# Kernel tuning notes

Hardware: AMD Instinct MI355X
Metric: run time of the kernel (lower is better)

Reference implementation:

```python
import jax, jax.numpy as jnp
import numpy as np

B, N, E, H = 8, 512, 256, 8
HD = E // H
FF = 4 * E
TOPK = max(1, int(N * 0.2))
FW_MAX_DIST = 10      # default of get_shortest_path_matrix
EMB_MAX_IDX = 6       # spd encoder: max_dist(5) + 1
LN_EPS = 1e-5


def _layernorm(x, g, b):
    m = jnp.mean(x, axis=-1, keepdims=True)
    v = jnp.var(x, axis=-1, keepdims=True)
    return (x - m) / jnp.sqrt(v + LN_EPS) * g + b


def setup_inputs() -> dict:
    key = jax.random.key(0)
    ks = jax.random.split(key, 12)
    s = 0.02
    return {
        "x": jax.random.normal(ks[0], (B, N, E), jnp.float32),
        "adj": jax.random.uniform(ks[1], (B, N, N), jnp.float32),
        "emb_spd": (jax.random.normal(ks[2], (EMB_MAX_IDX + 1, H), jnp.float32) * s),
        "w_qkv": jax.random.normal(ks[3], (3 * E, E), jnp.float32) * s,
        "b_qkv": jnp.zeros((3 * E,), jnp.float32),
        "w_out": jax.random.normal(ks[4], (E, E), jnp.float32) * s,
        "b_out": jnp.zeros((E,), jnp.float32),
        "w_ff1": jax.random.normal(ks[5], (FF, E), jnp.float32) * s,
        "b_ff1": jnp.zeros((FF,), jnp.float32),
        "w_ff2": jax.random.normal(ks[6], (E, FF), jnp.float32) * s,
        "b_ff2": jnp.zeros((E,), jnp.float32),
        "g1": jnp.ones((E,), jnp.float32),
        "beta1": jnp.zeros((E,), jnp.float32),
        "g2": jnp.ones((E,), jnp.float32),
        "beta2": jnp.zeros((E,), jnp.float32),
        "w_pool": jax.random.normal(ks[7], (1, E), jnp.float32) * s,
        "b_pool": jnp.zeros((1,), jnp.float32),
    }


def _combined_mask(adj, emb_spd):
    # top-k per row -> binary adjacency via scatter
    _, idx = jax.lax.top_k(adj, TOPK)                       # [B,N,k]
    bi = jnp.arange(B)[:, None, None]
    ri = jnp.arange(N)[None, :, None]
    binary = jnp.zeros_like(adj).at[bi, ri, idx].set(1.0)   # [B,N,N]

    # Floyd-Warshall shortest paths
    dist = jnp.where(binary == 1.0, 1.0, jnp.inf)
    ids = jnp.arange(N)
    dist = dist.at[:, ids, ids].set(0.0)

    def body(k, d):
        return jnp.minimum(d, d[:, :, k][:, :, None] + d[:, k, :][:, None, :])

    dist = jax.lax.fori_loop(0, N, body, dist)
    dist_i = jnp.where(dist > FW_MAX_DIST, -1.0, dist).astype(jnp.int32)

    # spatial bias embedding: indices = clamp(dist+1, 0, max_dist+1)
    sp_idx = jnp.clip(dist_i + 1, 0, EMB_MAX_IDX)           # [B,N,N]
    bias = jnp.transpose(emb_spd[sp_idx], (0, 3, 1, 2))     # [B,H,N,N]

    base = jnp.where(binary == 0.0, -jnp.inf, 0.0)[:, None] # [B,1,N,N]
    return base + bias                                      # [B,H,N,N]


def reference(x, adj, emb_spd, w_qkv, b_qkv, w_out, b_out,
              w_ff1, b_ff1, w_ff2, b_ff2, g1, beta1, g2, beta2,
              w_pool, b_pool):
    mask = _combined_mask(adj, emb_spd)                     # [B,H,N,N]

    # multi-head self-attention (PyTorch MHA, post-norm encoder layer, eval)
    qkv = x @ w_qkv.T + b_qkv                               # [B,N,3E]
    q, k, v = jnp.split(qkv, 3, axis=-1)
    q = q.reshape(B, N, H, HD).transpose(0, 2, 1, 3)
    k = k.reshape(B, N, H, HD).transpose(0, 2, 1, 3)
    v = v.reshape(B, N, H, HD).transpose(0, 2, 1, 3)
    scores = jnp.einsum("bhqd,bhkd->bhqk", q, k) / np.sqrt(HD) + mask
    attn = jax.nn.softmax(scores, axis=-1)
    ctx = jnp.einsum("bhqk,bhkd->bhqd", attn, v)
    ctx = ctx.transpose(0, 2, 1, 3).reshape(B, N, E)
    attn_out = ctx @ w_out.T + b_out

    x1 = _layernorm(x + attn_out, g1, beta1)
    ff = jax.nn.relu(x1 @ w_ff1.T + b_ff1) @ w_ff2.T + b_ff2
    x2 = _layernorm(x1 + ff, g2, beta2)

    # attention pooling over nodes
    w = jax.nn.softmax(jnp.tanh(x2 @ w_pool.T + b_pool), axis=1)  # [B,N,1]
    return jnp.sum(x2 * w, axis=1)                          # [B,E]
```

## Files before the change

kernel.cpp:

```cpp
#include <hip/hip_runtime.h>
#include <math.h>


#define B_ 8
#define N_ 512
#define E_ 256
#define H_ 8
#define HD_ 32
#define TOPK_ 102

typedef __attribute__((ext_vector_type(8))) short bf16x8;
typedef __attribute__((ext_vector_type(4))) float f32x4;

__device__ __forceinline__ unsigned short f2b(float f) {
  unsigned u = __builtin_bit_cast(unsigned, f);
  return (unsigned short)((u + 0x7FFFu + ((u >> 16) & 1u)) >> 16);
}

__global__ __launch_bounds__(256) void cvt_all(
    const float* __restrict__ x, const float* __restrict__ wqkv,
    const float* __restrict__ wout, const float* __restrict__ wff1,
    const float* __restrict__ wff2, unsigned short* __restrict__ xb,
    unsigned short* __restrict__ wqkvb, unsigned short* __restrict__ woutb,
    unsigned short* __restrict__ wff1b, unsigned short* __restrict__ wff2b) {
  int i = (blockIdx.x * 256 + threadIdx.x) * 4;
  const float* src;
  unsigned short* dst;
  int off;
  if (i < 1048576)      { src = x;    dst = xb;    off = i; }
  else if (i < 1245184) { src = wqkv; dst = wqkvb; off = i - 1048576; }
  else if (i < 1310720) { src = wout; dst = woutb; off = i - 1245184; }
  else if (i < 1572864) { src = wff1; dst = wff1b; off = i - 1310720; }
  else                  { src = wff2; dst = wff2b; off = i - 1572864; }
  float4 v = *(const float4*)(src + off);
  ushort4 o;
  o.x = f2b(v.x); o.y = f2b(v.y); o.z = f2b(v.z); o.w = f2b(v.w);
  *(ushort4*)(dst + off) = o;
}

__global__ __launch_bounds__(256) void topk_kernel(const float* __restrict__ adj,
                                                   unsigned int* __restrict__ bits) {
  const int row = blockIdx.x;
  const float* a = adj + (size_t)row * N_;
  __shared__ unsigned int hist[1024];
  __shared__ float cval[N_];
  __shared__ int cidx[N_];
  __shared__ int s_cnt;
  __shared__ int s_bb;
  __shared__ int s_need;
  __shared__ unsigned int rowbits[16];
  __shared__ int wsum[4];
  const int t = threadIdx.x;
  const int lane = t & 63;
  const int wave = t >> 6;

  hist[t] = 0u; hist[t + 256] = 0u; hist[t + 512] = 0u; hist[t + 768] = 0u;
  if (t == 0) s_cnt = 0;
  float v0 = a[t];
  float v1 = a[t + 256];
  __syncthreads();
  const int b0 = min(1023, max(0, (int)(v0 * 1024.0f)));
  const int b1 = min(1023, max(0, (int)(v1 * 1024.0f)));
  atomicAdd(&hist[b0], 1u);
  atomicAdd(&hist[b1], 1u);
  __syncthreads();
  const int base = 1020 - 4 * t;
  const int h0 = (int)hist[base], h1 = (int)hist[base + 1];
  const int h2 = (int)hist[base + 2], h3 = (int)hist[base + 3];
  const int g = h0 + h1 + h2 + h3;
  int sc = g;
  #pragma unroll
  for (int off = 1; off < 64; off <<= 1) {
    int y = __shfl_up(sc, off);
    sc += (lane >= off) ? y : 0;
  }
  if (lane == 63) wsum[wave] = sc;
  __syncthreads();
  int wo = 0;
  for (int w = 0; w < wave; w++) wo += wsum[w];
  const int incl = sc + wo;
  const int excl = incl - g;
  if (excl < TOPK_ && incl >= TOPK_) {
    int cum = excl;
    int bb = base;
    const int hh[4] = {h3, h2, h1, h0};
    const int bs[4] = {base + 3, base + 2, base + 1, base};
    #pragma unroll
    for (int u = 0; u < 4; u++) {
      if (cum + hh[u] >= TOPK_) { bb = bs[u]; break; }
      cum += hh[u];
    }
    s_bb = bb;
    s_need = TOPK_ - cum;
  }
  __syncthreads();
  const int bb = s_bb;
  const int need = s_need;
  const bool sel0 = (b0 > bb);
  const bool sel1 = (b1 > bb);
  if (b0 == bb) { int p = atomicAdd(&s_cnt, 1); cval[p] = v0; cidx[p] = t; }
  if (b1 == bb) { int p = atomicAdd(&s_cnt, 1); cval[p] = v1; cidx[p] = t + 256; }
  unsigned long long m0 = __ballot(sel0);
  unsigned long long m1 = __ballot(sel1);
  if (lane == 0) {
    rowbits[2 * wave + 0] = (unsigned int)m0;
    rowbits[2 * wave + 1] = (unsigned int)(m0 >> 32);
    rowbits[8 + 2 * wave + 0] = (unsigned int)m1;
    rowbits[8 + 2 * wave + 1] = (unsigned int)(m1 >> 32);
  }
  __syncthreads();
  const int cnt = s_cnt;
  for (int c = t; c < cnt; c += 256) {
    const float v = cval[c];
    const int idx = cidx[c];
    int r = 0;
    for (int j = 0; j < cnt; j++) {
      const float vj = cval[j];
      const int ij = cidx[j];
      if (vj > v || (vj == v && ij < idx)) r++;
    }
    if (r < need) atomicOr(&rowbits[idx >> 5], 1u << (idx & 31));
  }
  __syncthreads();
  if (t < 16) bits[(size_t)row * 16 + t] = rowbits[t];
}

__global__ __launch_bounds__(256) void gemm_mfma(
    const unsigned short* __restrict__ A, const unsigned short* __restrict__ W,
    const float* __restrict__ bias, const float* __restrict__ res,
    void* __restrict__ Cout, int M, int N, int K, int flags) {
  __shared__ __align__(16) unsigned short Af[8 * 64 * 8];
  __shared__ __align__(16) unsigned short Wf[8 * 64 * 8];
  const int tid = threadIdx.x;
  const int m0 = blockIdx.y * 64, n0 = blockIdx.x * 64;
  const int wave = tid >> 6, lane = tid & 63;
  const int wm = wave & 1, wn = wave >> 1;
  const int q = lane >> 4, l15 = lane & 15;
  const int r = tid >> 2, c0 = tid & 3;

  f32x4 acc[2][2];
  #pragma unroll
  for (int i = 0; i < 2; i++)
    #pragma unroll
    for (int j = 0; j < 2; j++) acc[i][j] = (f32x4){0.f, 0.f, 0.f, 0.f};

  const size_t arow = (size_t)(m0 + r) * K;
  const size_t wrow = (size_t)(n0 + r) * K;
  for (int k0 = 0; k0 < K; k0 += 64) {
    uint4 a0 = *(const uint4*)(A + arow + k0 + c0 * 8);
    uint4 a1 = *(const uint4*)(A + arow + k0 + (c0 + 4) * 8);
    uint4 w0 = *(const uint4*)(W + wrow + k0 + c0 * 8);
    uint4 w1 = *(const uint4*)(W + wrow + k0 + (c0 + 4) * 8);
    __syncthreads();
    {
      int kc = c0 >> 2, qq = c0 & 3;
      int s0 = ((r >> 4) * 2 + kc) * 64 + (r & 15) + qq * 16;
      int kc1 = (c0 + 4) >> 2, qq1 = (c0 + 4) & 3;
      int s1 = ((r >> 4) * 2 + kc1) * 64 + (r & 15) + qq1 * 16;
      *(uint4*)(Af + s0 * 8) = a0;
      *(uint4*)(Af + s1 * 8) = a1;
      *(uint4*)(Wf + s0 * 8) = w0;
      *(uint4*)(Wf + s1 * 8) = w1;
    }
    __syncthreads();
    #pragma unroll
    for (int kc = 0; kc < 2; kc++) {
      bf16x8 af[2], wf[2];
      #pragma unroll
      for (int mt = 0; mt < 2; mt++)
        af[mt] = *(const bf16x8*)(Af + (((wm * 2 + mt) * 2 + kc) * 64 + lane) * 8);
      #pragma unroll
      for (int nt = 0; nt < 2; nt++)
        wf[nt] = *(const bf16x8*)(Wf + (((wn * 2 + nt) * 2 + kc) * 64 + lane) * 8);
      #pragma unroll
      for (int mt = 0; mt < 2; mt++)
        #pragma unroll
        for (int nt = 0; nt < 2; nt++)
          acc[mt][nt] = __builtin_amdgcn_mfma_f32_16x16x32_bf16(af[mt], wf[nt], acc[mt][nt], 0, 0, 0);
    }
  }
  #pragma unroll
  for (int nt = 0; nt < 2; nt++) {
    const int col = n0 + (wn * 2 + nt) * 16 + l15;
    const float bv = bias[col];
    #pragma unroll
    for (int mt = 0; mt < 2; mt++) {
      const int rowb = m0 + (wm * 2 + mt) * 16 + q * 4;
      #pragma unroll
      for (int reg = 0; reg < 4; reg++) {
        const int row = rowb + reg;
        float o = acc[mt][nt][reg] + bv;
        if (res) o += res[(size_t)row * N + col];
        if (flags & 1) o = fmaxf(o, 0.f);
        if (flags & 2) ((unsigned short*)Cout)[(size_t)row * N + col] = f2b(o);
        else           ((float*)Cout)[(size_t)row * N + col] = o;
      }
    }
  }
}

__global__ __launch_bounds__(256) void attn_mfma(
    const unsigned short* __restrict__ qkv, const unsigned int* __restrict__ bits,
    const float* __restrict__ emb, unsigned short* __restrict__ ctxo) {
  const int bx = blockIdx.x;
  const int ib = bx & 7;
  const int h = (bx >> 3) & 7;
  const int b = bx >> 6;
  const int tid = threadIdx.x;
  const int lane = tid & 63;
  const int wave = tid >> 6;
  const int q = lane >> 4, l15 = lane & 15;

  __shared__ __align__(16) unsigned short kF[4 * 64 * 8];
  __shared__ __align__(16) unsigned short vF[4 * 64 * 8];
  __shared__ __align__(16) unsigned int mrow[64 * 16];
  __shared__ __align__(16) unsigned short pF[4][2 * 64 * 8];

  {
    int rr = tid >> 2, wq = tid & 3;
    uint4 mw = *(const uint4*)(bits + ((size_t)(b * N_ + ib * 64 + rr)) * 16 + wq * 4);
    *(uint4*)(mrow + rr * 16 + wq * 4) = mw;
  }
  const int i0w = ib * 64 + wave * 16;
  const bf16x8 qf = *(const bf16x8*)(qkv + ((size_t)(b * N_ + i0w + l15)) * 768 + h * HD_ + q * 8);
  const float delta = emb[1 * H_ + h] - emb[2 * H_ + h];
  const float scale = 0.17677669529663687f;

  float m_run[4], l_run[4];
  #pragma unroll
  for (int e = 0; e < 4; e++) { m_run[e] = -1e30f; l_run[e] = 0.f; }
  f32x4 cacc[2];
  cacc[0] = (f32x4){0.f, 0.f, 0.f, 0.f};
  cacc[1] = (f32x4){0.f, 0.f, 0.f, 0.f};

  unsigned short* pbase = &pF[wave][0];
  const int sj = tid >> 2, scb = tid & 3;

  #pragma unroll 1
  for (int jt = 0; jt < 8; jt++) {
    __syncthreads();
    {
      const unsigned short* kvrow = qkv + ((size_t)(b * N_ + jt * 64 + sj)) * 768 + h * HD_;
      uint4 kv4 = *(const uint4*)(kvrow + E_ + scb * 8);
      *(uint4*)(kF + (((sj >> 4) * 64) + (sj & 15) + scb * 16) * 8) = kv4;
      uint4 vv4 = *(const uint4*)(kvrow + 2 * E_ + scb * 8);
      const unsigned short* vp = (const unsigned short*)&vv4;
      #pragma unroll
      for (int e2 = 0; e2 < 8; e2++) {
        int d = scb * 8 + e2;
        int slot = ((d >> 4) * 2 + (sj >> 5)) * 64 + (d & 15) + ((sj >> 3) & 3) * 16;
        vF[slot * 8 + (sj & 7)] = vp[e2];
      }
    }
    __syncthreads();
    f32x4 s4[4];
    #pragma unroll
    for (int jtile = 0; jtile < 4; jtile++) {
      bf16x8 kf = *(const bf16x8*)(kF + (jtile * 64 + lane) * 8);
      s4[jtile] = __builtin_amdgcn_mfma_f32_16x16x32_bf16(qf, kf, (f32x4){0.f, 0.f, 0.f, 0.f}, 0, 0, 0);
    }
    unsigned long long mw64[4];
    #pragma unroll
    for (int reg = 0; reg < 4; reg++)
      mw64[reg] = *(const unsigned long long*)(mrow + (wave * 16 + q * 4 + reg) * 16 + jt * 2);
    float smat[4][4];
    #pragma unroll
    for (int jtile = 0; jtile < 4; jtile++) {
      #pragma unroll
      for (int reg = 0; reg < 4; reg++) {
        unsigned int w = (jtile & 2) ? (unsigned int)(mw64[reg] >> 32) : (unsigned int)mw64[reg];
        bool allowed = ((w >> ((jtile & 1) * 16 + l15)) & 1u) != 0u;
        int ig = ib * 64 + wave * 16 + q * 4 + reg;
        int jg = jt * 64 + jtile * 16 + l15;
        float s = s4[jtile][reg] * scale + ((jg == ig) ? delta : 0.f);
        smat[jtile][reg] = allowed ? s : -INFINITY;
      }
    }
    float alpha[4], pmat[4][4];
    #pragma unroll
    for (int reg = 0; reg < 4; reg++) {
      float mloc = fmaxf(fmaxf(smat[0][reg], smat[1][reg]), fmaxf(smat[2][reg], smat[3][reg]));
      #pragma unroll
      for (int off = 1; off < 16; off <<= 1) mloc = fmaxf(mloc, __shfl_xor(mloc, off));
      float mnew = fmaxf(m_run[reg], mloc);
      alpha[reg] = __expf(m_run[reg] - mnew);
      m_run[reg] = mnew;
      float ps = 0.f;
      #pragma unroll
      for (int jtile = 0; jtile < 4; jtile++) {
        float p = __expf(smat[jtile][reg] - mnew);
        pmat[jtile][reg] = p;
        ps += p;
      }
      #pragma unroll
      for (int off = 1; off < 16; off <<= 1) ps += __shfl_xor(ps, off);
      l_run[reg] = l_run[reg] * alpha[reg] + ps;
      cacc[0][reg] *= alpha[reg];
      cacc[1][reg] *= alpha[reg];
    }
    #pragma unroll
    for (int jtile = 0; jtile < 4; jtile++) {
      int j_l = jtile * 16 + l15;
      int sl = ((j_l >> 5) * 64 + ((j_l >> 3) & 3) * 16) * 8 + (j_l & 7);
      #pragma unroll
      for (int reg = 0; reg < 4; reg++)
        pbase[sl + (q * 4 + reg) * 8] = f2b(pmat[jtile][reg]);
    }
    #pragma unroll
    for (int kc = 0; kc < 2; kc++) {
      bf16x8 pf = *(const bf16x8*)(pbase + (kc * 64 + lane) * 8);
      #pragma unroll
      for (int dt = 0; dt < 2; dt++) {
        bf16x8 vf = *(const bf16x8*)(vF + ((dt * 2 + kc) * 64 + lane) * 8);
        cacc[dt] = __builtin_amdgcn_mfma_f32_16x16x32_bf16(pf, vf, cacc[dt], 0, 0, 0);
      }
    }
  }
  #pragma unroll
  for (int reg = 0; reg < 4; reg++) {
    const float linv = 1.f / l_run[reg];
    const size_t row = (size_t)(b * N_ + i0w + q * 4 + reg);
    #pragma unroll
    for (int dt = 0; dt < 2; dt++)
      ctxo[row * E_ + h * HD_ + dt * 16 + l15] = f2b(cacc[dt][reg] * linv);
  }
}

__global__ __launch_bounds__(256) void layernorm_kernel(
    const float* __restrict__ t, const float* __restrict__ g,
    const float* __restrict__ be, float* __restrict__ out,
    unsigned short* __restrict__ outb, const float* __restrict__ wp,
    const float* __restrict__ bp, float* __restrict__ ew) {
  const int row = blockIdx.x;
  const int tid = threadIdx.x;
  float v = t[(size_t)row * E_ + tid];
  float s = v, s2 = v * v;
  #pragma unroll
  for (int off = 32; off > 0; off >>= 1) {
    s += __shfl_xor(s, off);
    s2 += __shfl_xor(s2, off);
  }
  __shared__ float sh[8];
  const int wave = tid >> 6, lane = tid & 63;
  if (lane == 0) { sh[wave] = s; sh[4 + wave] = s2; }
  __syncthreads();
  s = sh[0] + sh[1] + sh[2] + sh[3];
  s2 = sh[4] + sh[5] + sh[6] + sh[7];
  float mean = s * (1.f / 256.f);
  float var = s2 * (1.f / 256.f) - mean * mean;
  float inv = rsqrtf(var + 1e-5f);
  float o = (v - mean) * inv * g[tid] + be[tid];
  out[(size_t)row * E_ + tid] = o;
  if (outb) outb[(size_t)row * E_ + tid] = f2b(o);
  if (ew) {
    float d = o * wp[tid];
    #pragma unroll
    for (int off = 32; off > 0; off >>= 1) d += __shfl_xor(d, off);
    __syncthreads();
    if (lane == 0) sh[wave] = d;
    __syncthreads();
    if (tid == 0) {
      float dot = sh[0] + sh[1] + sh[2] + sh[3] + bp[0];
      ew[row] = __expf(tanhf(dot));
    }
  }
}

__global__ __launch_bounds__(256) void pool_partial(
    const float* __restrict__ x2, const float* __restrict__ ew,
    float* __restrict__ partial, float* __restrict__ pwsum) {
  const int c = blockIdx.x;
  const int b = blockIdx.y;
  const int tid = threadIdx.x;
  const int r0 = b * N_ + c * 16;
  float acc = 0.f;
  #pragma unroll
  for (int n = 0; n < 16; n++)
    acc += ew[r0 + n] * x2[(size_t)(r0 + n) * E_ + tid];
  partial[(size_t)(b * 32 + c) * E_ + tid] = acc;
  if (tid < 16) {
    float w = ew[r0 + tid];
    #pragma unroll
    for (int off = 1; off < 16; off <<= 1) w += __shfl_xor(w, off);
    if (tid == 0) pwsum[b * 32 + c] = w;
  }
}

__global__ __launch_bounds__(256) void pool_final(
    const float* __restrict__ partial, const float* __restrict__ pwsum,
    float* __restrict__ out) {
  const int b = blockIdx.x;
  const int tid = threadIdx.x;
  float acc = 0.f, ws = 0.f;
  #pragma unroll
  for (int c = 0; c < 32; c++) acc += partial[(size_t)(b * 32 + c) * E_ + tid];
  #pragma unroll
  for (int c = 0; c < 32; c++) ws += pwsum[b * 32 + c];
  out[b * E_ + tid] = acc / ws;
}

extern "C" void kernel_launch(void* const* d_in, const int* in_sizes, int n_in,
                              void* d_out, int out_size, void* d_ws, size_t ws_size,
                              hipStream_t stream) {
  (void)in_sizes; (void)n_in; (void)out_size; (void)ws_size;
  const float* x      = (const float*)d_in[0];
  const float* adj    = (const float*)d_in[1];
  const float* emb    = (const float*)d_in[2];
  const float* w_qkv  = (const float*)d_in[3];
  const float* b_qkv  = (const float*)d_in[4];
  const float* w_out  = (const float*)d_in[5];
  const float* b_out  = (const float*)d_in[6];
  const float* w_ff1  = (const float*)d_in[7];
  const float* b_ff1  = (const float*)d_in[8];
  const float* w_ff2  = (const float*)d_in[9];
  const float* b_ff2  = (const float*)d_in[10];
  const float* g1     = (const float*)d_in[11];
  const float* be1    = (const float*)d_in[12];
  const float* g2     = (const float*)d_in[13];
  const float* be2    = (const float*)d_in[14];
  const float* w_pool = (const float*)d_in[15];
  const float* b_pool = (const float*)d_in[16];

  char* ws = (char*)d_ws;
  unsigned int*   bits  = (unsigned int*)ws;
  unsigned short* xb    = (unsigned short*)(ws + 262144);
  unsigned short* qkvb  = (unsigned short*)(ws + 2359296);
  unsigned short* hffb  = xb;
  unsigned short* ctxb  = (unsigned short*)(ws + 8650752);
  unsigned short* x1b   = (unsigned short*)(ws + 10747904);
  unsigned short* wqkvb = (unsigned short*)(ws + 12845056);
  unsigned short* woutb = (unsigned short*)(ws + 13238272);
  unsigned short* wff1b = (unsigned short*)(ws + 13369344);
  unsigned short* wff2b = (unsigned short*)(ws + 13893632);
  float*          tbuf  = (float*)(ws + 14417920);
  float*          x1    = (float*)(ws + 18612224);
  float*          x2    = (float*)(ws + 22806528);
  float*          ew      = (float*)(ws + 8650752);
  float*          partial = (float*)(ws + 8650752 + 16384);
  float*          pwsum   = (float*)(ws + 8650752 + 16384 + 262144);
  float*          outp  = (float*)d_out;

  const int M = B_ * N_;

  cvt_all<<<1835008 / 1024, 256, 0, stream>>>(x, w_qkv, w_out, w_ff1, w_ff2,
                                              xb, wqkvb, woutb, wff1b, wff2b);
  topk_kernel<<<B_ * N_, 256, 0, stream>>>(adj, bits);
  gemm_mfma<<<dim3(768 / 64, M / 64), 256, 0, stream>>>(
      xb, wqkvb, b_qkv, nullptr, qkvb, M, 768, E_, 2);
  attn_mfma<<<B_ * H_ * (N_ / 64), 256, 0, stream>>>(qkvb, bits, emb, ctxb);
  gemm_mfma<<<dim3(E_ / 64, M / 64), 256, 0, stream>>>(
      ctxb, woutb, b_out, x, tbuf, M, E_, E_, 0);
  layernorm_kernel<<<M, 256, 0, stream>>>(tbuf, g1, be1, x1, x1b,
                                          nullptr, nullptr, nullptr);
  gemm_mfma<<<dim3(1024 / 64, M / 64), 256, 0, stream>>>(
      x1b, wff1b, b_ff1, nullptr, hffb, M, 1024, E_, 1 | 2);
  gemm_mfma<<<dim3(E_ / 64, M / 64), 256, 0, stream>>>(
      hffb, wff2b, b_ff2, x1, tbuf, M, E_, 1024, 0);
  layernorm_kernel<<<M, 256, 0, stream>>>(tbuf, g2, be2, x2, nullptr,
                                          w_pool, b_pool, ew);
  pool_partial<<<dim3(32, 8), 256, 0, stream>>>(x2, ew, partial, pwsum);
  pool_final<<<B_, 256, 0, stream>>>(partial, pwsum, outp);
}
```

Measured before the change: 179.8 us.

## Fuse out-proj and FF2 GEMMs with layernorm; write transposed V from QKV GEMM

Replaces the out-projection and FF2 GEMMs and their separate layernorm kernels with a fused gemm_ln kernel. Each block computes 16 full rows of 256 columns with MFMA, reading operands straight from global memory, then does the row layernorm and pooling-weight dot in registers and shared memory. This removes the fp32 tbuf round trip and two kernel launches. The QKV GEMM now also writes V in a transposed per-head layout, so attention reads K and V fragments directly from global memory and drops its shared-memory staging and per-tile barriers. The trade-off is no LDS reuse in gemm_ln, only 256 small blocks, and more global-load traffic in attention.

```diff
diff --git a/kernel.cpp b/kernel.cpp
--- a/kernel.cpp
+++ b/kernel.cpp
@@ -128,7 +128,8 @@
 __global__ __launch_bounds__(256) void gemm_mfma(
     const unsigned short* __restrict__ A, const unsigned short* __restrict__ W,
     const float* __restrict__ bias, const float* __restrict__ res,
-    void* __restrict__ Cout, int M, int N, int K, int flags) {
+    void* __restrict__ Cout, unsigned short* __restrict__ vT,
+    int M, int N, int K, int flags) {
   __shared__ __align__(16) unsigned short Af[8 * 64 * 8];
   __shared__ __align__(16) unsigned short Wf[8 * 64 * 8];
   const int tid = threadIdx.x;
@@ -186,22 +187,35 @@
     #pragma unroll
     for (int mt = 0; mt < 2; mt++) {
       const int rowb = m0 + (wm * 2 + mt) * 16 + q * 4;
+      float ov[4];
       #pragma unroll
       for (int reg = 0; reg < 4; reg++) {
-        const int row = rowb + reg;
         float o = acc[mt][nt][reg] + bv;
-        if (res) o += res[(size_t)row * N + col];
+        if (res) o += res[(size_t)(rowb + reg) * N + col];
         if (flags & 1) o = fmaxf(o, 0.f);
-        if (flags & 2) ((unsigned short*)Cout)[(size_t)row * N + col] = f2b(o);
-        else           ((float*)Cout)[(size_t)row * N + col] = o;
+        ov[reg] = o;
       }
+      if (vT && col >= 512) {
+        const int d = (col - 512) & 31, hh2 = (col - 512) >> 5;
+        const int bidx = rowb >> 9, j0 = rowb & 511;
+        ushort4 st;
+        st.x = f2b(ov[0]); st.y = f2b(ov[1]); st.z = f2b(ov[2]); st.w = f2b(ov[3]);
+        *(ushort4*)(vT + ((size_t)((bidx * 8 + hh2) * 32 + d)) * 512 + j0) = st;
+      } else {
+        #pragma unroll
+        for (int reg = 0; reg < 4; reg++) {
+          if (flags & 2) ((unsigned short*)Cout)[(size_t)(rowb + reg) * N + col] = f2b(ov[reg]);
+          else           ((float*)Cout)[(size_t)(rowb + reg) * N + col] = ov[reg];
+        }
+      }
     }
   }
 }
 
 __global__ __launch_bounds__(256) void attn_mfma(
-    const unsigned short* __restrict__ qkv, const unsigned int* __restrict__ bits,
-    const float* __restrict__ emb, unsigned short* __restrict__ ctxo) {
+    const unsigned short* __restrict__ qkv, const unsigned short* __restrict__ vT,
+    const unsigned int* __restrict__ bits, const float* __restrict__ emb,
+    unsigned short* __restrict__ ctxo) {
   const int bx = blockIdx.x;
   const int ib = bx & 7;
   const int h = (bx >> 3) & 7;
@@ -211,8 +225,6 @@
   const int wave = tid >> 6;
   const int q = lane >> 4, l15 = lane & 15;
 
-  __shared__ __align__(16) unsigned short kF[4 * 64 * 8];
-  __shared__ __align__(16) unsigned short vF[4 * 64 * 8];
   __shared__ __align__(16) unsigned int mrow[64 * 16];
   __shared__ __align__(16) unsigned short pF[4][2 * 64 * 8];
 
@@ -221,6 +233,8 @@
     uint4 mw = *(const uint4*)(bits + ((size_t)(b * N_ + ib * 64 + rr)) * 16 + wq * 4);
     *(uint4*)(mrow + rr * 16 + wq * 4) = mw;
   }
+  __syncthreads();
+
   const int i0w = ib * 64 + wave * 16;
   const bf16x8 qf = *(const bf16x8*)(qkv + ((size_t)(b * N_ + i0w + l15)) * 768 + h * HD_ + q * 8);
   const float delta = emb[1 * H_ + h] - emb[2 * H_ + h];
@@ -234,29 +248,15 @@
   cacc[1] = (f32x4){0.f, 0.f, 0.f, 0.f};
 
   unsigned short* pbase = &pF[wave][0];
-  const int sj = tid >> 2, scb = tid & 3;
+  const unsigned short* kbase = qkv + (size_t)b * N_ * 768 + E_ + h * HD_ + q * 8;
+  const unsigned short* vbase = vT + ((size_t)((b * 8 + h) * 32 + l15)) * 512 + q * 8;
 
   #pragma unroll 1
   for (int jt = 0; jt < 8; jt++) {
-    __syncthreads();
-    {
-      const unsigned short* kvrow = qkv + ((size_t)(b * N_ + jt * 64 + sj)) * 768 + h * HD_;
-      uint4 kv4 = *(const uint4*)(kvrow + E_ + scb * 8);
-      *(uint4*)(kF + (((sj >> 4) * 64) + (sj & 15) + scb * 16) * 8) = kv4;
-      uint4 vv4 = *(const uint4*)(kvrow + 2 * E_ + scb * 8);
-      const unsigned short* vp = (const unsigned short*)&vv4;
-      #pragma unroll
-      for (int e2 = 0; e2 < 8; e2++) {
-        int d = scb * 8 + e2;
-        int slot = ((d >> 4) * 2 + (sj >> 5)) * 64 + (d & 15) + ((sj >> 3) & 3) * 16;
-        vF[slot * 8 + (sj & 7)] = vp[e2];
-      }
-    }
-    __syncthreads();
     f32x4 s4[4];
     #pragma unroll
     for (int jtile = 0; jtile < 4; jtile++) {
-      bf16x8 kf = *(const bf16x8*)(kF + (jtile * 64 + lane) * 8);
+      bf16x8 kf = *(const bf16x8*)(kbase + (size_t)(jt * 64 + jtile * 16 + l15) * 768);
       s4[jtile] = __builtin_amdgcn_mfma_f32_16x16x32_bf16(qf, kf, (f32x4){0.f, 0.f, 0.f, 0.f}, 0, 0, 0);
     }
     unsigned long long mw64[4];
@@ -311,7 +311,7 @@
       bf16x8 pf = *(const bf16x8*)(pbase + (kc * 64 + lane) * 8);
       #pragma unroll
       for (int dt = 0; dt < 2; dt++) {
-        bf16x8 vf = *(const bf16x8*)(vF + ((dt * 2 + kc) * 64 + lane) * 8);
+        bf16x8 vf = *(const bf16x8*)(vbase + (size_t)dt * 16 * 512 + jt * 64 + kc * 32);
         cacc[dt] = __builtin_amdgcn_mfma_f32_16x16x32_bf16(pf, vf, cacc[dt], 0, 0, 0);
       }
     }
@@ -326,42 +326,91 @@
   }
 }
 
-__global__ __launch_bounds__(256) void layernorm_kernel(
-    const float* __restrict__ t, const float* __restrict__ g,
-    const float* __restrict__ be, float* __restrict__ out,
-    unsigned short* __restrict__ outb, const float* __restrict__ wp,
-    const float* __restrict__ bp, float* __restrict__ ew) {
-  const int row = blockIdx.x;
+__global__ __launch_bounds__(256) void gemm_ln(
+    const unsigned short* __restrict__ A, const unsigned short* __restrict__ W,
+    const float* __restrict__ bias, const float* __restrict__ res,
+    const float* __restrict__ g, const float* __restrict__ be,
+    float* __restrict__ xout, unsigned short* __restrict__ xbout,
+    const float* __restrict__ wp, const float* __restrict__ bp,
+    float* __restrict__ ew, int K) {
   const int tid = threadIdx.x;
-  float v = t[(size_t)row * E_ + tid];
-  float s = v, s2 = v * v;
-  #pragma unroll
-  for (int off = 32; off > 0; off >>= 1) {
-    s += __shfl_xor(s, off);
-    s2 += __shfl_xor(s2, off);
-  }
-  __shared__ float sh[8];
-  const int wave = tid >> 6, lane = tid & 63;
-  if (lane == 0) { sh[wave] = s; sh[4 + wave] = s2; }
-  __syncthreads();
-  s = sh[0] + sh[1] + sh[2] + sh[3];
-  s2 = sh[4] + sh[5] + sh[6] + sh[7];
-  float mean = s * (1.f / 256.f);
-  float var = s2 * (1.f / 256.f) - mean * mean;
-  float inv = rsqrtf(var + 1e-5f);
-  float o = (v - mean) * inv * g[tid] + be[tid];
-  out[(size_t)row * E_ + tid] = o;
-  if (outb) outb[(size_t)row * E_ + tid] = f2b(o);
+  const int wv = tid >> 6, lane = tid & 63;
+  const int q = lane >> 4, l15 = lane & 15;
+  const int m0 = blockIdx.x * 16;
+  f32x4 acc[4];
+  #pragma unroll
+  for (int nt = 0; nt < 4; nt++) acc[nt] = (f32x4){0.f, 0.f, 0.f, 0.f};
+
+  const unsigned short* ap = A + (size_t)(m0 + l15) * K + q * 8;
+  const unsigned short* wr = W + (size_t)(wv * 64 + l15) * K + q * 8;
+  const int K32 = K >> 5;
+  for (int kc = 0; kc < K32; kc++) {
+    bf16x8 af = *(const bf16x8*)(ap + kc * 32);
+    #pragma unroll
+    for (int nt = 0; nt < 4; nt++) {
+      bf16x8 wf = *(const bf16x8*)(wr + (size_t)nt * 16 * K + kc * 32);
+      acc[nt] = __builtin_amdgcn_mfma_f32_16x16x32_bf16(af, wf, acc[nt], 0, 0, 0);
+    }
+  }
+  __shared__ float rs[16][4], rs2[16][4];
+  float o[4][4];
+  int cols[4];
+  #pragma unroll
+  for (int nt = 0; nt < 4; nt++) cols[nt] = wv * 64 + nt * 16 + l15;
+  #pragma unroll
+  for (int reg = 0; reg < 4; reg++) {
+    const int row = m0 + q * 4 + reg;
+    float p = 0.f, p2 = 0.f;
+    #pragma unroll
+    for (int nt = 0; nt < 4; nt++) {
+      float v = acc[nt][reg] + bias[cols[nt]];
+      if (res) v += res[(size_t)row * 256 + cols[nt]];
+      o[nt][reg] = v;
+      p += v; p2 += v * v;
+    }
+    #pragma unroll
+    for (int off = 1; off < 16; off <<= 1) {
+      p += __shfl_xor(p, off);
+      p2 += __shfl_xor(p2, off);
+    }
+    if (l15 == 0) { rs[q * 4 + reg][wv] = p; rs2[q * 4 + reg][wv] = p2; }
+  }
+  __syncthreads();
+  #pragma unroll
+  for (int reg = 0; reg < 4; reg++) {
+    const int r = q * 4 + reg;
+    float s = rs[r][0] + rs[r][1] + rs[r][2] + rs[r][3];
+    float s2 = rs2[r][0] + rs2[r][1] + rs2[r][2] + rs2[r][3];
+    float mean = s * (1.f / 256.f);
+    float var = s2 * (1.f / 256.f) - mean * mean;
+    float inv = rsqrtf(var + 1e-5f);
+    #pragma unroll
+    for (int nt = 0; nt < 4; nt++) {
+      float on = (o[nt][reg] - mean) * inv * g[cols[nt]] + be[cols[nt]];
+      o[nt][reg] = on;
+      xout[(size_t)(m0 + r) * 256 + cols[nt]] = on;
+      if (xbout) xbout[(size_t)(m0 + r) * 256 + cols[nt]] = f2b(on);
+    }
+  }
   if (ew) {
-    float d = o * wp[tid];
-    #pragma unroll
-    for (int off = 32; off > 0; off >>= 1) d += __shfl_xor(d, off);
     __syncthreads();
-    if (lane == 0) sh[wave] = d;
+    #pragma unroll
+    for (int reg = 0; reg < 4; reg++) {
+      float d = 0.f;
+      #pragma unroll
+      for (int nt = 0; nt < 4; nt++) d += o[nt][reg] * wp[cols[nt]];
+      #pragma unroll
+      for (int off = 1; off < 16; off <<= 1) d += __shfl_xor(d, off);
+      if (l15 == 0) rs[q * 4 + reg][wv] = d;
+    }
     __syncthreads();
-    if (tid == 0) {
-      float dot = sh[0] + sh[1] + sh[2] + sh[3] + bp[0];
-      ew[row] = __expf(tanhf(dot));
+    if (wv == 0 && l15 == 0) {
+      #pragma unroll
+      for (int reg = 0; reg < 4; reg++) {
+        const int r = q * 4 + reg;
+        float dot = rs[r][0] + rs[r][1] + rs[r][2] + rs[r][3] + bp[0];
+        ew[m0 + r] = __expf(tanhf(dot));
+      }
     }
   }
 }
@@ -432,7 +481,7 @@
   unsigned short* woutb = (unsigned short*)(ws + 13238272);
   unsigned short* wff1b = (unsigned short*)(ws + 13369344);
   unsigned short* wff2b = (unsigned short*)(ws + 13893632);
-  float*          tbuf  = (float*)(ws + 14417920);
+  unsigned short* vTb   = (unsigned short*)(ws + 14417920);
   float*          x1    = (float*)(ws + 18612224);
   float*          x2    = (float*)(ws + 22806528);
   float*          ew      = (float*)(ws + 8650752);
@@ -446,18 +495,14 @@
                                               xb, wqkvb, woutb, wff1b, wff2b);
   topk_kernel<<<B_ * N_, 256, 0, stream>>>(adj, bits);
   gemm_mfma<<<dim3(768 / 64, M / 64), 256, 0, stream>>>(
-      xb, wqkvb, b_qkv, nullptr, qkvb, M, 768, E_, 2);
-  attn_mfma<<<B_ * H_ * (N_ / 64), 256, 0, stream>>>(qkvb, bits, emb, ctxb);
-  gemm_mfma<<<dim3(E_ / 64, M / 64), 256, 0, stream>>>(
-      ctxb, woutb, b_out, x, tbuf, M, E_, E_, 0);
-  layernorm_kernel<<<M, 256, 0, stream>>>(tbuf, g1, be1, x1, x1b,
-                                          nullptr, nullptr, nullptr);
+      xb, wqkvb, b_qkv, nullptr, qkvb, vTb, M, 768, E_, 2);
+  attn_mfma<<<B_ * H_ * (N_ / 64), 256, 0, stream>>>(qkvb, vTb, bits, emb, ctxb);
+  gemm_ln<<<M / 16, 256, 0, stream>>>(ctxb, woutb, b_out, x, g1, be1,
+                                      x1, x1b, nullptr, nullptr, nullptr, E_);
   gemm_mfma<<<dim3(1024 / 64, M / 64), 256, 0, stream>>>(
-      x1b, wff1b, b_ff1, nullptr, hffb, M, 1024, E_, 1 | 2);
-  gemm_mfma<<<dim3(E_ / 64, M / 64), 256, 0, stream>>>(
-      hffb, wff2b, b_ff2, x1, tbuf, M, E_, 1024, 0);
-  layernorm_kernel<<<M, 256, 0, stream>>>(tbuf, g2, be2, x2, nullptr,
-                                          w_pool, b_pool, ew);
+      x1b, wff1b, b_ff1, nullptr, hffb, nullptr, M, 1024, E_, 1 | 2);
+  gemm_ln<<<M / 16, 256, 0, stream>>>(hffb, wff2b, b_ff2, x1, g2, be2,
+                                      x2, nullptr, w_pool, b_pool, ew, 1024);
   pool_partial<<<dim3(32, 8), 256, 0, stream>>>(x2, ew, partial, pwsum);
   pool_final<<<B_, 256, 0, stream>>>(partial, pwsum, outp);
 }
```

After: 193.3 us. +7.5%, slower.

## Emit K/V in MFMA fragment layout from QKV GEMM; drop attention LDS staging

Applied to the files above, without the earlier changes.

The QKV GEMM epilogue now writes K and V columns straight into global buffers laid out in the MFMA fragment order the attention kernel consumes. The attention kernel reads its K/V fragments directly from global memory with vector loads, which removes the per-tile LDS staging, the scalar V transpose and the two barriers per key tile. In exchange the GEMM epilogue does scattered, narrow stores, and each of the 8 query blocks per head rereads K/V from global memory or cache instead of from shared memory.

```diff
diff --git a/kernel.cpp b/kernel.cpp
--- a/kernel.cpp
+++ b/kernel.cpp
@@ -128,7 +128,8 @@
 __global__ __launch_bounds__(256) void gemm_mfma(
     const unsigned short* __restrict__ A, const unsigned short* __restrict__ W,
     const float* __restrict__ bias, const float* __restrict__ res,
-    void* __restrict__ Cout, int M, int N, int K, int flags) {
+    void* __restrict__ Cout, unsigned short* __restrict__ kG,
+    unsigned short* __restrict__ vG, int M, int N, int K, int flags) {
   __shared__ __align__(16) unsigned short Af[8 * 64 * 8];
   __shared__ __align__(16) unsigned short Wf[8 * 64 * 8];
   const int tid = threadIdx.x;
@@ -186,21 +187,48 @@
     #pragma unroll
     for (int mt = 0; mt < 2; mt++) {
       const int rowb = m0 + (wm * 2 + mt) * 16 + q * 4;
+      float ov[4];
       #pragma unroll
       for (int reg = 0; reg < 4; reg++) {
-        const int row = rowb + reg;
         float o = acc[mt][nt][reg] + bv;
-        if (res) o += res[(size_t)row * N + col];
+        if (res) o += res[(size_t)(rowb + reg) * N + col];
         if (flags & 1) o = fmaxf(o, 0.f);
-        if (flags & 2) ((unsigned short*)Cout)[(size_t)row * N + col] = f2b(o);
-        else           ((float*)Cout)[(size_t)row * N + col] = o;
+        ov[reg] = o;
       }
+      if (kG && col >= 256 && col < 512) {
+        const int dfull = col - 256;
+        const int hh2 = dfull >> 5, d = dfull & 31;
+        const int q2 = d >> 3, sub = d & 7;
+        const int bidx = rowb >> 9, j = rowb & 511;
+        const int jt = j >> 6, jtile = (j >> 4) & 3, jl = j & 15;
+        unsigned short* kp = kG +
+            ((size_t)(((bidx * 8 + hh2) * 8 + jt) * 4 + jtile) * 64 + q2 * 16 + jl) * 8 + sub;
+        kp[0] = f2b(ov[0]); kp[8] = f2b(ov[1]); kp[16] = f2b(ov[2]); kp[24] = f2b(ov[3]);
+      } else if (vG && col >= 512) {
+        const int dfull = col - 512;
+        const int hh2 = dfull >> 5, d = dfull & 31;
+        const int dt = d >> 4, dl = d & 15;
+        const int bidx = rowb >> 9, j = rowb & 511;
+        const int jt = j >> 6, jj = j & 63;
+        const int kc = jj >> 5, q2 = (jj >> 3) & 3, sub0 = jj & 7;
+        ushort4 st;
+        st.x = f2b(ov[0]); st.y = f2b(ov[1]); st.z = f2b(ov[2]); st.w = f2b(ov[3]);
+        *(ushort4*)(vG +
+            ((size_t)(((bidx * 8 + hh2) * 8 + jt) * 4 + dt * 2 + kc) * 64 + q2 * 16 + dl) * 8 + sub0) = st;
+      } else {
+        #pragma unroll
+        for (int reg = 0; reg < 4; reg++) {
+          if (flags & 2) ((unsigned short*)Cout)[(size_t)(rowb + reg) * N + col] = f2b(ov[reg]);
+          else           ((float*)Cout)[(size_t)(rowb + reg) * N + col] = ov[reg];
+        }
+      }
     }
   }
 }
 
 __global__ __launch_bounds__(256) void attn_mfma(
-    const unsigned short* __restrict__ qkv, const unsigned int* __restrict__ bits,
+    const unsigned short* __restrict__ qkv, const unsigned short* __restrict__ kG,
+    const unsigned short* __restrict__ vG, const unsigned int* __restrict__ bits,
     const float* __restrict__ emb, unsigned short* __restrict__ ctxo) {
   const int bx = blockIdx.x;
   const int ib = bx & 7;
@@ -211,8 +239,6 @@
   const int wave = tid >> 6;
   const int q = lane >> 4, l15 = lane & 15;
 
-  __shared__ __align__(16) unsigned short kF[4 * 64 * 8];
-  __shared__ __align__(16) unsigned short vF[4 * 64 * 8];
   __shared__ __align__(16) unsigned int mrow[64 * 16];
   __shared__ __align__(16) unsigned short pF[4][2 * 64 * 8];
 
@@ -221,6 +247,8 @@
     uint4 mw = *(const uint4*)(bits + ((size_t)(b * N_ + ib * 64 + rr)) * 16 + wq * 4);
     *(uint4*)(mrow + rr * 16 + wq * 4) = mw;
   }
+  __syncthreads();
+
   const int i0w = ib * 64 + wave * 16;
   const bf16x8 qf = *(const bf16x8*)(qkv + ((size_t)(b * N_ + i0w + l15)) * 768 + h * HD_ + q * 8);
   const float delta = emb[1 * H_ + h] - emb[2 * H_ + h];
@@ -234,29 +262,15 @@
   cacc[1] = (f32x4){0.f, 0.f, 0.f, 0.f};
 
   unsigned short* pbase = &pF[wave][0];
-  const int sj = tid >> 2, scb = tid & 3;
+  const unsigned short* kb = kG + (size_t)(b * 8 + h) * 8 * 4 * 512;
+  const unsigned short* vb = vG + (size_t)(b * 8 + h) * 8 * 4 * 512;
 
   #pragma unroll 1
   for (int jt = 0; jt < 8; jt++) {
-    __syncthreads();
-    {
-      const unsigned short* kvrow = qkv + ((size_t)(b * N_ + jt * 64 + sj)) * 768 + h * HD_;
-      uint4 kv4 = *(const uint4*)(kvrow + E_ + scb * 8);
-      *(uint4*)(kF + (((sj >> 4) * 64) + (sj & 15) + scb * 16) * 8) = kv4;
-      uint4 vv4 = *(const uint4*)(kvrow + 2 * E_ + scb * 8);
-      const unsigned short* vp = (const unsigned short*)&vv4;
-      #pragma unroll
-      for (int e2 = 0; e2 < 8; e2++) {
-        int d = scb * 8 + e2;
-        int slot = ((d >> 4) * 2 + (sj >> 5)) * 64 + (d & 15) + ((sj >> 3) & 3) * 16;
-        vF[slot * 8 + (sj & 7)] = vp[e2];
-      }
-    }
-    __syncthreads();
     f32x4 s4[4];
     #pragma unroll
     for (int jtile = 0; jtile < 4; jtile++) {
-      bf16x8 kf = *(const bf16x8*)(kF + (jtile * 64 + lane) * 8);
+      bf16x8 kf = *(const bf16x8*)(kb + (size_t)(jt * 4 + jtile) * 512 + lane * 8);
       s4[jtile] = __builtin_amdgcn_mfma_f32_16x16x32_bf16(qf, kf, (f32x4){0.f, 0.f, 0.f, 0.f}, 0, 0, 0);
     }
     unsigned long long mw64[4];
@@ -311,7 +325,7 @@
       bf16x8 pf = *(const bf16x8*)(pbase + (kc * 64 + lane) * 8);
       #pragma unroll
       for (int dt = 0; dt < 2; dt++) {
-        bf16x8 vf = *(const bf16x8*)(vF + ((dt * 2 + kc) * 64 + lane) * 8);
+        bf16x8 vf = *(const bf16x8*)(vb + (size_t)(jt * 4 + dt * 2 + kc) * 512 + lane * 8);
         cacc[dt] = __builtin_amdgcn_mfma_f32_16x16x32_bf16(pf, vf, cacc[dt], 0, 0, 0);
       }
     }
@@ -432,9 +446,11 @@
   unsigned short* woutb = (unsigned short*)(ws + 13238272);
   unsigned short* wff1b = (unsigned short*)(ws + 13369344);
   unsigned short* wff2b = (unsigned short*)(ws + 13893632);
-  float*          tbuf  = (float*)(ws + 14417920);
-  float*          x1    = (float*)(ws + 18612224);
-  float*          x2    = (float*)(ws + 22806528);
+  unsigned short* vG    = (unsigned short*)(ws + 14417920);
+  unsigned short* kG    = (unsigned short*)(ws + 16515072);
+  float*          tbuf  = (float*)(ws + 18612224);
+  float*          x1    = (float*)(ws + 22806528);
+  float*          x2    = (float*)(ws + 27000832);
   float*          ew      = (float*)(ws + 8650752);
   float*          partial = (float*)(ws + 8650752 + 16384);
   float*          pwsum   = (float*)(ws + 8650752 + 16384 + 262144);
@@ -446,16 +462,16 @@
                                               xb, wqkvb, woutb, wff1b, wff2b);
   topk_kernel<<<B_ * N_, 256, 0, stream>>>(adj, bits);
   gemm_mfma<<<dim3(768 / 64, M / 64), 256, 0, stream>>>(
-      xb, wqkvb, b_qkv, nullptr, qkvb, M, 768, E_, 2);
-  attn_mfma<<<B_ * H_ * (N_ / 64), 256, 0, stream>>>(qkvb, bits, emb, ctxb);
+      xb, wqkvb, b_qkv, nullptr, qkvb, kG, vG, M, 768, E_, 2);
+  attn_mfma<<<B_ * H_ * (N_ / 64), 256, 0, stream>>>(qkvb, kG, vG, bits, emb, ctxb);
   gemm_mfma<<<dim3(E_ / 64, M / 64), 256, 0, stream>>>(
-      ctxb, woutb, b_out, x, tbuf, M, E_, E_, 0);
+      ctxb, woutb, b_out, x, tbuf, nullptr, nullptr, M, E_, E_, 0);
   layernorm_kernel<<<M, 256, 0, stream>>>(tbuf, g1, be1, x1, x1b,
                                           nullptr, nullptr, nullptr);
   gemm_mfma<<<dim3(1024 / 64, M / 64), 256, 0, stream>>>(
-      x1b, wff1b, b_ff1, nullptr, hffb, M, 1024, E_, 1 | 2);
+      x1b, wff1b, b_ff1, nullptr, hffb, nullptr, nullptr, M, 1024, E_, 1 | 2);
   gemm_mfma<<<dim3(E_ / 64, M / 64), 256, 0, stream>>>(
-      hffb, wff2b, b_ff2, x1, tbuf, M, E_, 1024, 0);
+      hffb, wff2b, b_ff2, x1, tbuf, nullptr, nullptr, M, E_, 1024, 0);
   layernorm_kernel<<<M, 256, 0, stream>>>(tbuf, g2, be2, x2, nullptr,
                                           w_pool, b_pool, ew);
   pool_partial<<<dim3(32, 8), 256, 0, stream>>>(x2, ew, partial, pwsum);
```

After: 177.5 us. Within noise of the previous version (-1.3%).
